# Optimization experiments

Measured on AMD Instinct MI355X. Metric: run time of the kernel, lower is better.

Reference implementation:

```python
import jax, jax.numpy as jnp
import numpy as np

N = 50000   # num nodes
E = 800000  # num edges (avg degree 16)
D = 64      # feature dim for input and both layers


def setup_inputs() -> dict:
    key = jax.random.key(0)
    ks = jax.random.split(key, 8)
    x = jax.random.normal(ks[0], (N, D), dtype=jnp.float32)
    edge_index = jax.random.randint(ks[1], (2, E), 0, N, dtype=jnp.int32)
    s = 1.0 / np.sqrt(D)
    # PyG SAGEConv params per layer: lin_l (on aggregated neighbors, with bias),
    # lin_r (on root node, no bias)
    Wl0 = jax.random.uniform(ks[2], (D, D), jnp.float32, -s, s)
    bl0 = jax.random.uniform(ks[3], (D,), jnp.float32, -s, s)
    Wr0 = jax.random.uniform(ks[4], (D, D), jnp.float32, -s, s)
    Wl1 = jax.random.uniform(ks[5], (D, D), jnp.float32, -s, s)
    bl1 = jax.random.uniform(ks[6], (D,), jnp.float32, -s, s)
    Wr1 = jax.random.uniform(ks[7], (D, D), jnp.float32, -s, s)
    return dict(node_features=x, edge_index=edge_index,
                Wl0=Wl0, bl0=bl0, Wr0=Wr0, Wl1=Wl1, bl1=bl1, Wr1=Wr1)


def _sage_conv(x, src, dst, Wl, bl, Wr):
    """PyG SAGEConv (mean aggr) after add_self_loops: mean over neighbors+self."""
    msg = x[src]  # [E, D] irregular gather
    summ = jax.ops.segment_sum(msg, dst, num_segments=x.shape[0]) + x  # self-loop
    deg = jax.ops.segment_sum(jnp.ones(src.shape, x.dtype), dst,
                              num_segments=x.shape[0]) + 1.0
    mean = summ / deg[:, None]
    return mean @ Wl + bl + x @ Wr


def reference(node_features, edge_index, Wl0, bl0, Wr0, Wl1, bl1, Wr1):
    src, dst = edge_index[0], edge_index[1]
    # dropout is a no-op in eval mode; batch_norms are unused in the original forward
    x = jax.nn.relu(_sage_conv(node_features, src, dst, Wl0, bl0, Wr0))
    x = jax.nn.relu(_sage_conv(x, src, dst, Wl1, bl1, Wr1))
    return x
```

## Files before the change

### kernel.cpp

```cpp
#include <hip/hip_runtime.h>
#include <hip/hip_bf16.h>

#define N_NODES 50000
#define N_EDGES 800000
#define FDIM 64
#define NBUCK 196
#define CAP 4608
#define CAP2 5632
#define PAD 16

typedef __attribute__((ext_vector_type(8))) short short8;
typedef __attribute__((ext_vector_type(4))) float f32x4;

__device__ __forceinline__ unsigned f2bf(float f) {
    unsigned u = __float_as_uint(f);
    u += 0x7fffu + ((u >> 16) & 1u);
    return u >> 16;
}
__device__ __forceinline__ float bf2f_lo(unsigned u) { return __uint_as_float(u << 16); }
__device__ __forceinline__ float bf2f_hi(unsigned u) { return __uint_as_float(u & 0xffff0000u); }

__device__ __forceinline__ int excl_scan_256(int v, int* wtot, int* wincl) {
    const int t = threadIdx.x, lane = t & 63, w = t >> 6;
    int sv = v;
#pragma unroll
    for (int off = 1; off < 64; off <<= 1) {
        int u = __shfl_up(sv, off, 64);
        if (lane >= off) sv += u;
    }
    if (lane == 63) wtot[w] = sv;
    __syncthreads();
    if (w == 0 && lane < 4) {
        int incl = 0;
#pragma unroll
        for (int k = 0; k < 4; ++k)
            if (k <= lane) incl += wtot[k];
        wincl[lane] = incl;
    }
    __syncthreads();
    return (w ? wincl[w - 1] : 0) + sv - v;
}

__global__ __launch_bounds__(256)
void preprocess_kernel(const float* __restrict__ x0, unsigned short* __restrict__ x_bf,
                       const float* __restrict__ Wl0, const float* __restrict__ Wr0,
                       const float* __restrict__ Wl1, const float* __restrict__ Wr1,
                       unsigned short* __restrict__ pW,
                       const int* __restrict__ src, const int* __restrict__ dst,
                       int* __restrict__ cur_pad, unsigned* __restrict__ ebuf) {
    const int b = blockIdx.x;
    const int t = threadIdx.x;
    if (b < 3125) {
        int i = (b * 256 + t) * 4;
        float4 v = *(const float4*)(x0 + i);
        uint2 o;
        o.x = f2bf(v.x) | (f2bf(v.y) << 16);
        o.y = f2bf(v.z) | (f2bf(v.w) << 16);
        *(uint2*)(x_bf + i) = o;
    } else if (b < 3129) {
        const float* Wsrc[4] = {Wl0, Wr0, Wl1, Wr1};
        const float* W = Wsrc[b - 3125];
        unsigned short* P = pW + (b - 3125) * FDIM * FDIM;
        for (int idx = t; idx < FDIM * FDIM; idx += 256) {
            int j = idx & 7;
            int lane = (idx >> 3) & 63;
            int g = idx >> 9;
            int ct = g >> 1, kk = g & 1;
            int k = kk * 32 + ((lane >> 4) & 3) * 8 + j;
            int col = ct * 16 + (lane & 15);
            P[idx] = (unsigned short)f2bf(W[k * FDIM + col]);
        }
    } else {
        __shared__ int h[NBUCK];
        __shared__ int base[NBUCK];
        if (t < NBUCK) h[t] = 0;
        __syncthreads();

        int e0 = (b - 3129) * 1024;
        int bk[4], rk[4]; unsigned pk[4];
#pragma unroll
        for (int k = 0; k < 4; ++k) {
            int e = e0 + k * 256 + t;
            if (e < N_EDGES) {
                int d = dst[e];
                bk[k] = d >> 8;
                pk[k] = ((unsigned)d << 16) | (unsigned)src[e];
                rk[k] = atomicAdd(&h[bk[k]], 1);
            } else bk[k] = -1;
        }
        __syncthreads();
        if (t < NBUCK) {
            int c = h[t];
            base[t] = c ? (t * CAP + atomicAdd(&cur_pad[t * PAD], c)) : 0;
        }
        __syncthreads();
#pragma unroll
        for (int k = 0; k < 4; ++k)
            if (bk[k] >= 0) ebuf[base[bk[k]] + rk[k]] = pk[k];
    }
}

__global__ __launch_bounds__(256)
void bucket_csr_kernel(const unsigned* __restrict__ ebuf, const int* __restrict__ cur_pad,
                       int* __restrict__ row_start, unsigned short* __restrict__ degs,
                       unsigned short* __restrict__ csr) {
    __shared__ int cnt[256];
    __shared__ int cur[256];
    __shared__ int wtot[4], wincl[4];
    const int b = blockIdx.x;
    const int t = threadIdx.x;
    const int s = b * CAP;
    const int e = s + cur_pad[b * PAD];
    const int s2 = b * CAP2;

    cnt[t] = 0;
    __syncthreads();
    for (int i = s + t; i < e; i += 256)
        atomicAdd(&cnt[(ebuf[i] >> 16) & 255], 1);
    __syncthreads();

    int c = cnt[t];
    int c8 = (c + 7) & ~7;
    int ex = excl_scan_256(c8, wtot, wincl);
    cur[t] = ex;
    int node = b * 256 + t;
    if (node < N_NODES) {
        row_start[node] = s2 + ex;
        degs[node] = (unsigned short)c;
    }
    __syncthreads();

    for (int i = s + t; i < e; i += 256) {
        unsigned pk = ebuf[i];
        int pos = s2 + atomicAdd(&cur[(pk >> 16) & 255], 1);
        csr[pos] = (unsigned short)pk;
    }
}

template <bool OUT_BF16>
__global__ __launch_bounds__(128)
void sage_fused_kernel(const unsigned short* __restrict__ xb,
                       const int* __restrict__ row_start,
                       const unsigned short* __restrict__ degs,
                       const unsigned short* __restrict__ csr,
                       const unsigned short* __restrict__ pWl,
                       const float* __restrict__ bl,
                       const unsigned short* __restrict__ pWr,
                       float* __restrict__ out_f32,
                       unsigned short* __restrict__ out_bf) {
    __shared__ __align__(16) unsigned short smean[16][FDIM];
    __shared__ __align__(16) unsigned short sxs[16][FDIM];

    const int w = threadIdx.x >> 6;
    const int lane = threadIdx.x & 63;
    const int slot = lane >> 3;
    const int c = lane & 7;
    const int base = blockIdx.x * 16;
    const int r = w * 8 + slot;
    const int n = base + r;

    uint4 sv = *(const uint4*)(xb + (size_t)n * FDIM + c * 8);

    const int rs = row_start[n];
    const int deg = degs[n];
    const int po = (c ^ (r & 7)) * 8;

    *(uint4*)(&sxs[r][po]) = sv;
    float s0 = bf2f_lo(sv.x), s1 = bf2f_hi(sv.x);
    float s2 = bf2f_lo(sv.y), s3 = bf2f_hi(sv.y);
    float s4 = bf2f_lo(sv.z), s5 = bf2f_hi(sv.z);
    float s6 = bf2f_lo(sv.w), s7 = bf2f_hi(sv.w);

#define ACC(v_) do {                                   \
        s0 += bf2f_lo(v_.x); s1 += bf2f_hi(v_.x);      \
        s2 += bf2f_lo(v_.y); s3 += bf2f_hi(v_.y);      \
        s4 += bf2f_lo(v_.z); s5 += bf2f_hi(v_.z);      \
        s6 += bf2f_lo(v_.w); s7 += bf2f_hi(v_.w);      \
    } while (0)

    int idx = rs;
    int rem = deg;
    while (rem >= 8) {
        uint4 iA = *(const uint4*)(csr + idx);
        int a0 = iA.x & 0xffff, a1 = iA.x >> 16;
        int a2 = iA.y & 0xffff, a3 = iA.y >> 16;
        int a4 = iA.z & 0xffff, a5 = iA.z >> 16;
        int a6 = iA.w & 0xffff, a7 = iA.w >> 16;
        uint4 v0 = *(const uint4*)(xb + (size_t)a0 * FDIM + c * 8);
        uint4 v1 = *(const uint4*)(xb + (size_t)a1 * FDIM + c * 8);
        uint4 v2 = *(const uint4*)(xb + (size_t)a2 * FDIM + c * 8);
        uint4 v3 = *(const uint4*)(xb + (size_t)a3 * FDIM + c * 8);
        uint4 v4 = *(const uint4*)(xb + (size_t)a4 * FDIM + c * 8);
        uint4 v5 = *(const uint4*)(xb + (size_t)a5 * FDIM + c * 8);
        uint4 v6 = *(const uint4*)(xb + (size_t)a6 * FDIM + c * 8);
        uint4 v7 = *(const uint4*)(xb + (size_t)a7 * FDIM + c * 8);
        ACC(v0); ACC(v1); ACC(v2); ACC(v3);
        ACC(v4); ACC(v5); ACC(v6); ACC(v7);
        idx += 8; rem -= 8;
    }
    if (rem > 0) {
        uint4 iA = *(const uint4*)(csr + idx);
        int a[8];
        a[0] = iA.x & 0xffff; a[1] = iA.x >> 16;
        a[2] = iA.y & 0xffff; a[3] = iA.y >> 16;
        a[4] = iA.z & 0xffff; a[5] = iA.z >> 16;
        a[6] = iA.w & 0xffff; a[7] = iA.w >> 16;
#pragma unroll
        for (int k = 0; k < 8; ++k) {
            if (k < rem) {
                uint4 v = *(const uint4*)(xb + (size_t)a[k] * FDIM + c * 8);
                ACC(v);
            }
        }
    }
#undef ACC

    const float inv = 1.0f / (float)(deg + 1);
    uint4 o;
    o.x = f2bf(s0 * inv) | (f2bf(s1 * inv) << 16);
    o.y = f2bf(s2 * inv) | (f2bf(s3 * inv) << 16);
    o.z = f2bf(s4 * inv) | (f2bf(s5 * inv) << 16);
    o.w = f2bf(s6 * inv) | (f2bf(s7 * inv) << 16);
    *(uint4*)(&smean[r][po]) = o;
    __syncthreads();

    const int qq = lane >> 4;
    const int rr = lane & 15;

    short8 am0 = *(const short8*)(&smean[rr][((0 + qq) ^ (rr & 7)) * 8]);
    short8 am1 = *(const short8*)(&smean[rr][((4 + qq) ^ (rr & 7)) * 8]);
    short8 ax0 = *(const short8*)(&sxs[rr][((0 + qq) ^ (rr & 7)) * 8]);
    short8 ax1 = *(const short8*)(&sxs[rr][((4 + qq) ^ (rr & 7)) * 8]);

    const short8* pl = (const short8*)pWl;
    const short8* pr = (const short8*)pWr;

#pragma unroll
    for (int tk = 0; tk < 2; ++tk) {
        const int ct = w * 2 + tk;
        short8 bl0v = pl[(ct * 2 + 0) * 64 + lane];
        short8 bl1v = pl[(ct * 2 + 1) * 64 + lane];
        short8 br0v = pr[(ct * 2 + 0) * 64 + lane];
        short8 br1v = pr[(ct * 2 + 1) * 64 + lane];

        float b = bl[ct * 16 + rr];
        f32x4 acc = {b, b, b, b};
        acc = __builtin_amdgcn_mfma_f32_16x16x32_bf16(am0, bl0v, acc, 0, 0, 0);
        acc = __builtin_amdgcn_mfma_f32_16x16x32_bf16(am1, bl1v, acc, 0, 0, 0);
        acc = __builtin_amdgcn_mfma_f32_16x16x32_bf16(ax0, br0v, acc, 0, 0, 0);
        acc = __builtin_amdgcn_mfma_f32_16x16x32_bf16(ax1, br1v, acc, 0, 0, 0);

#pragma unroll
        for (int reg = 0; reg < 4; ++reg) {
            int node = base + qq * 4 + reg;
            float v = fmaxf(acc[reg], 0.0f);
            if (OUT_BF16) out_bf[(size_t)node * FDIM + ct * 16 + rr] = (unsigned short)f2bf(v);
            else          out_f32[(size_t)node * FDIM + ct * 16 + rr] = v;
        }
    }
}

extern "C" void kernel_launch(void* const* d_in, const int* in_sizes, int n_in,
                              void* d_out, int out_size, void* d_ws, size_t ws_size,
                              hipStream_t stream) {
    const float* x0  = (const float*)d_in[0];
    const int*   ei  = (const int*)d_in[1];
    const float* Wl0 = (const float*)d_in[2];
    const float* bl0 = (const float*)d_in[3];
    const float* Wr0 = (const float*)d_in[4];
    const float* Wl1 = (const float*)d_in[5];
    const float* bl1 = (const float*)d_in[6];
    const float* Wr1 = (const float*)d_in[7];
    float* out = (float*)d_out;

    const int* src = ei;
    const int* dst = ei + N_EDGES;

    int* cur_pad    = (int*)d_ws;
    int* row_start  = cur_pad + 3136;
    unsigned short* degs = (unsigned short*)(row_start + 50000);
    unsigned* ebuf  = (unsigned*)(degs + 50000);
    unsigned short* csr_u16 = (unsigned short*)(ebuf + NBUCK * CAP);
    unsigned short* x_bf = csr_u16 + (NBUCK * CAP2 + 1024);
    unsigned short* h_bf = x_bf + (size_t)N_NODES * FDIM;
    unsigned short* pW   = h_bf + (size_t)N_NODES * FDIM;

    hipMemsetAsync(cur_pad, 0, 3136 * sizeof(int), stream);
    preprocess_kernel<<<3911, 256, 0, stream>>>(x0, x_bf, Wl0, Wr0, Wl1, Wr1,
                                                pW, src, dst, cur_pad, ebuf);
    bucket_csr_kernel<<<NBUCK, 256, 0, stream>>>(ebuf, cur_pad, row_start, degs, csr_u16);

    sage_fused_kernel<true><<<N_NODES / 16, 128, 0, stream>>>(
        x_bf, row_start, degs, csr_u16, pW + 0 * FDIM * FDIM, bl0,
        pW + 1 * FDIM * FDIM, nullptr, h_bf);
    sage_fused_kernel<false><<<N_NODES / 16, 128, 0, stream>>>(
        h_bf, row_start, degs, csr_u16, pW + 2 * FDIM * FDIM, bl1,
        pW + 3 * FDIM * FDIM, out, nullptr);
}
```

Before: 153.3 us.

## Vectorize edge binning loads, stage CSR in LDS, prefetch neighbor indices

The edge binning step now loads src/dst as int4 vectors per thread instead of strided scalar loads. The CSR build keeps bucket edges in registers across both passes, scatters them into a shared-memory buffer, and then writes that buffer out with coalesced 16-byte stores instead of scattered 2-byte global writes. In the aggregation loop, the next group of eight neighbor indices is loaded before the current gathers are accumulated, hiding index-load latency. The costs are higher register pressure (18 packed values per thread) and about 11 KB of extra LDS per block in the CSR kernel.

Measured after the change: 150.7 us. No clear change (-1.7%).

```diff
diff --git a/kernel.cpp b/kernel.cpp
--- a/kernel.cpp
+++ b/kernel.cpp
@@ -76,17 +76,22 @@
         if (t < NBUCK) h[t] = 0;
         __syncthreads();
 
-        int e0 = (b - 3129) * 1024;
-        int bk[4], rk[4]; unsigned pk[4];
-#pragma unroll
-        for (int k = 0; k < 4; ++k) {
-            int e = e0 + k * 256 + t;
-            if (e < N_EDGES) {
-                int d = dst[e];
-                bk[k] = d >> 8;
-                pk[k] = ((unsigned)d << 16) | (unsigned)src[e];
-                rk[k] = atomicAdd(&h[bk[k]], 1);
-            } else bk[k] = -1;
+        int e0 = (b - 3129) * 1024 + t * 4;
+        int bk0 = -1, bk1 = -1, bk2 = -1, bk3 = -1;
+        int rk0 = 0, rk1 = 0, rk2 = 0, rk3 = 0;
+        unsigned pk0 = 0, pk1 = 0, pk2 = 0, pk3 = 0;
+        const bool ok = (e0 < N_EDGES);
+        if (ok) {
+            int4 s4 = *(const int4*)(src + e0);
+            int4 d4 = *(const int4*)(dst + e0);
+            bk0 = d4.x >> 8; pk0 = ((unsigned)d4.x << 16) | (unsigned)s4.x;
+            bk1 = d4.y >> 8; pk1 = ((unsigned)d4.y << 16) | (unsigned)s4.y;
+            bk2 = d4.z >> 8; pk2 = ((unsigned)d4.z << 16) | (unsigned)s4.z;
+            bk3 = d4.w >> 8; pk3 = ((unsigned)d4.w << 16) | (unsigned)s4.w;
+            rk0 = atomicAdd(&h[bk0], 1);
+            rk1 = atomicAdd(&h[bk1], 1);
+            rk2 = atomicAdd(&h[bk2], 1);
+            rk3 = atomicAdd(&h[bk3], 1);
         }
         __syncthreads();
         if (t < NBUCK) {
@@ -94,9 +99,12 @@
             base[t] = c ? (t * CAP + atomicAdd(&cur_pad[t * PAD], c)) : 0;
         }
         __syncthreads();
-#pragma unroll
-        for (int k = 0; k < 4; ++k)
-            if (bk[k] >= 0) ebuf[base[bk[k]] + rk[k]] = pk[k];
+        if (ok) {
+            ebuf[base[bk0] + rk0] = pk0;
+            ebuf[base[bk1] + rk1] = pk1;
+            ebuf[base[bk2] + rk2] = pk2;
+            ebuf[base[bk3] + rk3] = pk3;
+        }
     }
 }
 
@@ -107,16 +115,25 @@
     __shared__ int cnt[256];
     __shared__ int cur[256];
     __shared__ int wtot[4], wincl[4];
+    __shared__ __align__(16) unsigned short sC[CAP2];
     const int b = blockIdx.x;
     const int t = threadIdx.x;
     const int s = b * CAP;
-    const int e = s + cur_pad[b * PAD];
+    const int m = cur_pad[b * PAD];
     const int s2 = b * CAP2;
 
     cnt[t] = 0;
     __syncthreads();
-    for (int i = s + t; i < e; i += 256)
-        atomicAdd(&cnt[(ebuf[i] >> 16) & 255], 1);
+
+    unsigned pk[18];
+#pragma unroll
+    for (int k = 0; k < 18; ++k) {
+        int i = k * 256 + t;
+        if (i < m) {
+            pk[k] = ebuf[s + i];
+            atomicAdd(&cnt[(pk[k] >> 16) & 255], 1);
+        }
+    }
     __syncthreads();
 
     int c = cnt[t];
@@ -130,11 +147,19 @@
     }
     __syncthreads();
 
-    for (int i = s + t; i < e; i += 256) {
-        unsigned pk = ebuf[i];
-        int pos = s2 + atomicAdd(&cur[(pk >> 16) & 255], 1);
-        csr[pos] = (unsigned short)pk;
-    }
+#pragma unroll
+    for (int k = 0; k < 18; ++k) {
+        int i = k * 256 + t;
+        if (i < m) {
+            int pos = atomicAdd(&cur[(pk[k] >> 16) & 255], 1);
+            sC[pos] = (unsigned short)pk[k];
+        }
+    }
+    __syncthreads();
+
+    const int tot = wincl[3];
+    for (int i = t * 8; i < tot; i += 2048)
+        *(uint4*)(csr + s2 + i) = *(const uint4*)(&sC[i]);
 }
 
 template <bool OUT_BF16>
@@ -180,8 +205,8 @@
 
     int idx = rs;
     int rem = deg;
+    uint4 iA = *(const uint4*)(csr + idx);
     while (rem >= 8) {
-        uint4 iA = *(const uint4*)(csr + idx);
         int a0 = iA.x & 0xffff, a1 = iA.x >> 16;
         int a2 = iA.y & 0xffff, a3 = iA.y >> 16;
         int a4 = iA.z & 0xffff, a5 = iA.z >> 16;
@@ -194,12 +219,13 @@
         uint4 v5 = *(const uint4*)(xb + (size_t)a5 * FDIM + c * 8);
         uint4 v6 = *(const uint4*)(xb + (size_t)a6 * FDIM + c * 8);
         uint4 v7 = *(const uint4*)(xb + (size_t)a7 * FDIM + c * 8);
+        if (rem > 8)
+            iA = *(const uint4*)(csr + idx + 8);
         ACC(v0); ACC(v1); ACC(v2); ACC(v3);
         ACC(v4); ACC(v5); ACC(v6); ACC(v7);
         idx += 8; rem -= 8;
     }
     if (rem > 0) {
-        uint4 iA = *(const uint4*)(csr + idx);
         int a[8];
         a[0] = iA.x & 0xffff; a[1] = iA.x >> 16;
         a[2] = iA.y & 0xffff; a[3] = iA.y >> 16;
```
